# Performance work log

Measured on AMD Instinct MI355X. Metric: run time of the kernel, lower is better.

## Reference

```python
import jax, jax.numpy as jnp
import numpy as np

N = 1024      # n_nodes
S = 32        # state_dim
M = 32        # message_dim
STEPS = 5     # n_steps


def setup_inputs() -> dict:
    key = jax.random.key(0)
    ks = jax.random.split(key, 12)
    w = lambda k, shape: jax.random.normal(k, shape, jnp.float32) * 0.02
    return {
        "J": jax.random.normal(ks[0], (N, N), jnp.float32),
        "b": jax.random.normal(ks[1], (N,), jnp.float32),
        # message_passing MLP (Linear(2S+3->M), Linear(M->M), Linear(M->M))
        "W1": w(ks[2], (M, 2 * S + 3)), "b1": jnp.zeros((M,), jnp.float32),
        "W2": w(ks[3], (M, M)),         "b2": jnp.zeros((M,), jnp.float32),
        "W3": w(ks[4], (M, M)),         "b3": jnp.zeros((M,), jnp.float32),
        # GRU(input=S+M, hidden=S). h0 is always zero in the original forward,
        # so weight_hh never contributes (only bias_hh does) and is omitted.
        "W_ih": w(ks[5], (3 * S, S + M)),
        "b_ih": w(ks[6], (3 * S,)),
        "b_hh": w(ks[7], (3 * S,)),
        # readout MLP (Linear(S->M), Linear(M->M), Linear(M->2))
        "R1": w(ks[8], (M, S)),  "rb1": jnp.zeros((M,), jnp.float32),
        "R2": w(ks[9], (M, M)),  "rb2": jnp.zeros((M,), jnp.float32),
        "R3": w(ks[10], (2, M)), "rb3": jnp.zeros((2,), jnp.float32),
    }


def reference(J, b, W1, b1, W2, b2, W3, b3, W_ih, b_ih, b_hh, R1, rb1, R2, rb2, R3, rb3):
    # Split first linear over the concat [h_i, h_j, J_ij, b_i, b_j] so the
    # [N, N, 2S+3] concat tensor is never materialized.
    W1a, W1b = W1[:, :S], W1[:, S:2 * S]
    wJ, wbi, wbj = W1[:, 2 * S], W1[:, 2 * S + 1], W1[:, 2 * S + 2]

    def step(h, _):
        hi = h @ W1a.T                       # [N, M] (sender part)
        hj = h @ W1b.T                       # [N, M] (receiver part)
        pre = (hi[:, None, :] + hj[None, :, :]
               + J[:, :, None] * wJ
               + b[:, None, None] * wbi
               + b[None, :, None] * wbj
               + b1)                          # [N, N, M]
        x = jax.nn.relu(pre)
        x = jax.nn.relu(x @ W2.T + b2)
        x = jax.nn.relu(x @ W3.T + b3)       # message_i_j: [N, N, M]
        m = x.sum(0)                          # message to node j: sum over senders i
        # GRU with zero initial hidden state: h' = (1-z) * n_gate
        gi = jnp.concatenate([h, m], axis=-1) @ W_ih.T + b_ih  # [N, 3S]
        r = jax.nn.sigmoid(gi[:, :S] + b_hh[:S])
        z = jax.nn.sigmoid(gi[:, S:2 * S] + b_hh[S:2 * S])
        n = jnp.tanh(gi[:, 2 * S:] + r * b_hh[2 * S:])
        return (1.0 - z) * n, None

    h0 = jnp.zeros((N, S), J.dtype)
    h, _ = jax.lax.scan(step, h0, None, length=STEPS)

    r = jax.nn.relu(h @ R1.T + rb1)
    r = jax.nn.relu(r @ R2.T + rb2)
    r = jax.nn.relu(r @ R3.T + rb3)          # [N, 2]
    return jax.nn.sigmoid(r)
```

## Files before the change

### kernel.cpp

```cpp
#include <hip/hip_runtime.h>
#include <math.h>

#define NN 1024

typedef __attribute__((ext_vector_type(8))) short bf16x8;
typedef __attribute__((ext_vector_type(4))) float f32x4;
typedef __attribute__((ext_vector_type(4))) unsigned int u32x4;

__device__ __forceinline__ float sigmoidf_(float x) { return 1.0f / (1.0f + __expf(-x)); }

__device__ __forceinline__ unsigned int pk_bf16(float a, float b) {
    unsigned int ua = __float_as_uint(a), ub = __float_as_uint(b);
    ua += 0x7fffu + ((ua >> 16) & 1u);
    ub += 0x7fffu + ((ub >> 16) & 1u);
    return (ua >> 16) | (ub & 0xffff0000u);
}
__device__ __forceinline__ unsigned short f2bf_rne(float a) {
    unsigned int ua = __float_as_uint(a);
    ua += 0x7fffu + ((ua >> 16) & 1u);
    return (unsigned short)(ua >> 16);
}

struct Ctx {
    bf16x8 w2a0, w2a1, w3a0, w3a1;
    f32x4 b2v0, b2v1, b3v0, b3v1;
    float wj8[8];
};

__device__ __forceinline__ void make_ctx(Ctx& c, int p, int q,
    const float* __restrict__ W1, const float* __restrict__ W2,
    const float* __restrict__ b2, const float* __restrict__ W3,
    const float* __restrict__ b3)
{
    union FU { bf16x8 v; unsigned short s[8]; } t0, t1, t2, t3;
#pragma unroll
    for (int jj = 0; jj < 8; jj++) {
        int k = q * 8 + jj;
        t0.s[jj] = f2bf_rne(W2[p * 32 + k]);
        t1.s[jj] = f2bf_rne(W2[(16 + p) * 32 + k]);
        t2.s[jj] = f2bf_rne(W3[p * 32 + k]);
        t3.s[jj] = f2bf_rne(W3[(16 + p) * 32 + k]);
        c.wj8[jj] = W1[k * 67 + 64];
    }
    c.w2a0 = t0.v; c.w2a1 = t1.v; c.w3a0 = t2.v; c.w3a1 = t3.v;
#pragma unroll
    for (int r = 0; r < 4; r++) {
        c.b2v0[r] = b2[q * 4 + r];  c.b2v1[r] = b2[16 + q * 4 + r];
        c.b3v0[r] = b3[q * 4 + r];  c.b3v1[r] = b3[16 + q * 4 + r];
    }
}

__global__ __launch_bounds__(256) void k_pre(
    const float* __restrict__ J, const float* __restrict__ b,
    const float* __restrict__ W1, const float* __restrict__ b1,
    float* __restrict__ Jt, float* __restrict__ h,
    float* __restrict__ u0, float* __restrict__ v)
{
    __shared__ float tile[32][33];
    const int t = blockIdx.x;
    const int tid = threadIdx.x;
    if (t < 1024) {
        int tx = (t & 31) * 32, ty = (t >> 5) * 32;
        int x = tid & 31, y = tid >> 5;
#pragma unroll
        for (int r = 0; r < 4; r++)
            tile[y + 8 * r][x] = J[(size_t)(ty + y + 8 * r) * NN + tx + x];
        __syncthreads();
#pragma unroll
        for (int r = 0; r < 4; r++)
            Jt[(size_t)(tx + y + 8 * r) * NN + ty + x] = tile[x][y + 8 * r];
    } else {
        int idx = (t - 1024) * 256 + tid;
        int row = idx >> 5, mm = idx & 31;
        float bi = b[row];
        h[idx]  = 0.f;
        u0[idx] = bi * W1[mm * 67 + 65];
        v[idx]  = fmaf(bi, W1[mm * 67 + 66], b1[mm]);
    }
}

__global__ __launch_bounds__(256, 4) void k_step(
    const float* __restrict__ Jt, const float* __restrict__ W1,
    const float* __restrict__ W2, const float* __restrict__ b2,
    const float* __restrict__ W3, const float* __restrict__ b3,
    const float* __restrict__ Wih, const float* __restrict__ bih,
    const float* __restrict__ bhh, const float* __restrict__ b,
    const float* __restrict__ b1,
    const float* __restrict__ R1, const float* __restrict__ rb1,
    const float* __restrict__ R2, const float* __restrict__ rb2,
    const float* __restrict__ R3, const float* __restrict__ rb3,
    float* __restrict__ h, float* __restrict__ v,
    const float* __restrict__ ui, float* __restrict__ uo,
    float* __restrict__ out, int do_out)
{
    __shared__ float red[4 * 32];
    __shared__ float hm[64];
    __shared__ float gbuf[96];
    __shared__ float hnb[32];
    __shared__ float tb[32];

    const int tid = threadIdx.x;
    const int w = tid >> 6;
    const int l = tid & 63;
    const int p = l & 15;
    const int q = l >> 4;
    const int j = blockIdx.x & 1023;
    const bool primary = (blockIdx.x < 1024);

    Ctx c; make_ctx(c, p, q, W1, W2, b2, W3, b3);
    const float* Jtrow = Jt + (size_t)j * NN;

    float vv[8];
#pragma unroll
    for (int jj = 0; jj < 8; jj++) vv[jj] = v[j * 32 + q * 8 + jj];

    const int s0 = (p | ((l & 16) << 1)) << 2;
    const int s1 = s0 + 64;
    const bool qlo = (l & 32) == 0;

    f32x4 acc0 = {0.f, 0.f, 0.f, 0.f}, acc1 = {0.f, 0.f, 0.f, 0.f};

    const int ibase = w * 256;
    float  jwA = Jtrow[ibase + p];
    float4 uaA = *(const float4*)(ui + (ibase + p) * 32 + q * 8);
    float4 ubA = *(const float4*)(ui + (ibase + p) * 32 + q * 8 + 4);
    float  jwB = Jtrow[ibase + 16 + p];
    float4 uaB = *(const float4*)(ui + (ibase + 16 + p) * 32 + q * 8);
    float4 ubB = *(const float4*)(ui + (ibase + 16 + p) * 32 + q * 8 + 4);

#pragma unroll 4
    for (int t = 0; t < 16; ++t) {
        float  jw_c;
        float4 ua_c, ub_c;
        if ((t & 1) == 0) { jw_c = jwA; ua_c = uaA; ub_c = ubA; }
        else              { jw_c = jwB; ua_c = uaB; ub_c = ubB; }
        if (t < 14) {
            const int in = ibase + (t + 2) * 16 + p;
            if ((t & 1) == 0) {
                jwA = Jtrow[in];
                uaA = *(const float4*)(ui + in * 32 + q * 8);
                ubA = *(const float4*)(ui + in * 32 + q * 8 + 4);
            } else {
                jwB = Jtrow[in];
                uaB = *(const float4*)(ui + in * 32 + q * 8);
                ubB = *(const float4*)(ui + in * 32 + q * 8 + 4);
            }
        }

        float xr[8];
        xr[0] = fmaxf(fmaf(jw_c, c.wj8[0], ua_c.x + vv[0]), 0.f);
        xr[1] = fmaxf(fmaf(jw_c, c.wj8[1], ua_c.y + vv[1]), 0.f);
        xr[2] = fmaxf(fmaf(jw_c, c.wj8[2], ua_c.z + vv[2]), 0.f);
        xr[3] = fmaxf(fmaf(jw_c, c.wj8[3], ua_c.w + vv[3]), 0.f);
        xr[4] = fmaxf(fmaf(jw_c, c.wj8[4], ub_c.x + vv[4]), 0.f);
        xr[5] = fmaxf(fmaf(jw_c, c.wj8[5], ub_c.y + vv[5]), 0.f);
        xr[6] = fmaxf(fmaf(jw_c, c.wj8[6], ub_c.z + vv[6]), 0.f);
        xr[7] = fmaxf(fmaf(jw_c, c.wj8[7], ub_c.w + vv[7]), 0.f);

        union BU { u32x4 u4; bf16x8 v; unsigned int d[4]; } bx;
#pragma unroll
        for (int cc = 0; cc < 4; cc++) bx.d[cc] = pk_bf16(xr[2 * cc], xr[2 * cc + 1]);

        f32x4 c0 = __builtin_amdgcn_mfma_f32_16x16x32_bf16(c.w2a0, bx.v, c.b2v0, 0, 0, 0);
        f32x4 c1 = __builtin_amdgcn_mfma_f32_16x16x32_bf16(c.w2a1, bx.v, c.b2v1, 0, 0, 0);

        const int d0 = (int)pk_bf16(fmaxf(c0[0], 0.f), fmaxf(c0[1], 0.f));
        const int d1 = (int)pk_bf16(fmaxf(c0[2], 0.f), fmaxf(c0[3], 0.f));
        const int d2 = (int)pk_bf16(fmaxf(c1[0], 0.f), fmaxf(c1[1], 0.f));
        const int d3 = (int)pk_bf16(fmaxf(c1[2], 0.f), fmaxf(c1[3], 0.f));

        const int A0 = __builtin_amdgcn_ds_bpermute(s0, d0);
        const int A1 = __builtin_amdgcn_ds_bpermute(s0, d1);
        const int A2 = __builtin_amdgcn_ds_bpermute(s1, d0);
        const int A3 = __builtin_amdgcn_ds_bpermute(s1, d1);
        const int B0 = __builtin_amdgcn_ds_bpermute(s0, d2);
        const int B1 = __builtin_amdgcn_ds_bpermute(s0, d3);
        const int B2 = __builtin_amdgcn_ds_bpermute(s1, d2);
        const int B3 = __builtin_amdgcn_ds_bpermute(s1, d3);

        union BU yr;
        yr.d[0] = (unsigned)(qlo ? A0 : B0);
        yr.d[1] = (unsigned)(qlo ? A1 : B1);
        yr.d[2] = (unsigned)(qlo ? A2 : B2);
        yr.d[3] = (unsigned)(qlo ? A3 : B3);

        f32x4 e0 = __builtin_amdgcn_mfma_f32_16x16x32_bf16(c.w3a0, yr.v, c.b3v0, 0, 0, 0);
        f32x4 e1 = __builtin_amdgcn_mfma_f32_16x16x32_bf16(c.w3a1, yr.v, c.b3v1, 0, 0, 0);
#pragma unroll
        for (int r = 0; r < 4; r++) {
            acc0[r] += fmaxf(e0[r], 0.f);
            acc1[r] += fmaxf(e1[r], 0.f);
        }
    }

#pragma unroll
    for (int bit = 1; bit < 16; bit <<= 1) {
#pragma unroll
        for (int r = 0; r < 4; r++) {
            acc0[r] += __shfl_xor(acc0[r], bit);
            acc1[r] += __shfl_xor(acc1[r], bit);
        }
    }
    if (p == 0) {
#pragma unroll
        for (int r = 0; r < 4; r++) {
            red[w * 32 + q * 4 + r]      = acc0[r];
            red[w * 32 + 16 + q * 4 + r] = acc1[r];
        }
    }

    if (!primary) return;
    __syncthreads();

    if (tid < 64) {
        float val;
        if (tid < 32) val = h[j * 32 + tid];
        else {
            int s = tid - 32;
            val = red[s] + red[32 + s] + red[64 + s] + red[96 + s];
        }
        hm[tid] = val;
    }
    __syncthreads();

    if (tid < 192) {
        const int row = tid >> 1, half = tid & 1;
        const float* wr = Wih + row * 64 + half * 32;
        const float* hh = hm + half * 32;
        float acc = 0.f;
#pragma unroll
        for (int k4 = 0; k4 < 8; k4++) {
            float4 w4 = *(const float4*)(wr + 4 * k4);
            acc = fmaf(w4.x, hh[4 * k4 + 0], acc);
            acc = fmaf(w4.y, hh[4 * k4 + 1], acc);
            acc = fmaf(w4.z, hh[4 * k4 + 2], acc);
            acc = fmaf(w4.w, hh[4 * k4 + 3], acc);
        }
        acc += __shfl_xor(acc, 1);
        if (half == 0) gbuf[row] = acc + bih[row];
    }
    __syncthreads();

    if (tid < 32) {
        const int s = tid;
        float r = sigmoidf_(gbuf[s] + bhh[s]);
        float z = sigmoidf_(gbuf[32 + s] + bhh[32 + s]);
        float n = tanhf(gbuf[64 + s] + r * bhh[64 + s]);
        float hn_ = (1.0f - z) * n;
        hnb[s] = hn_;
        h[j * 32 + s] = hn_;
    }
    __syncthreads();

    if (tid < 64) {
        const int s = tid & 31;
        const bool isV = tid >= 32;
        const float bj = b[j];
        const float* wr = W1 + s * 67 + (isV ? 32 : 0);
        float acc = isV ? fmaf(bj, W1[s * 67 + 66], b1[s]) : bj * W1[s * 67 + 65];
#pragma unroll
        for (int k = 0; k < 32; k++) acc = fmaf(wr[k], hnb[k], acc);
        if (isV) v[j * 32 + s] = acc;
        else     uo[j * 32 + s] = acc;
    }

    if (do_out) {
        __syncthreads();
        if (tid < 32) {
            float a = rb1[tid];
            const float* rr = R1 + tid * 32;
#pragma unroll
            for (int k4 = 0; k4 < 8; k4++) {
                float4 w4 = *(const float4*)(rr + 4 * k4);
                a = fmaf(w4.x, hnb[4 * k4 + 0], a);
                a = fmaf(w4.y, hnb[4 * k4 + 1], a);
                a = fmaf(w4.z, hnb[4 * k4 + 2], a);
                a = fmaf(w4.w, hnb[4 * k4 + 3], a);
            }
            gbuf[tid] = fmaxf(a, 0.f);
        }
        __syncthreads();
        if (tid < 32) {
            float a = rb2[tid];
            const float* rr = R2 + tid * 32;
#pragma unroll
            for (int k4 = 0; k4 < 8; k4++) {
                float4 w4 = *(const float4*)(rr + 4 * k4);
                a = fmaf(w4.x, gbuf[4 * k4 + 0], a);
                a = fmaf(w4.y, gbuf[4 * k4 + 1], a);
                a = fmaf(w4.z, gbuf[4 * k4 + 2], a);
                a = fmaf(w4.w, gbuf[4 * k4 + 3], a);
            }
            tb[tid] = fmaxf(a, 0.f);
        }
        __syncthreads();
        if (tid < 2) {
            float a = rb3[tid];
            const float* rr = R3 + tid * 32;
#pragma unroll
            for (int k = 0; k < 32; k++) a = fmaf(rr[k], tb[k], a);
            out[j * 2 + tid] = sigmoidf_(fmaxf(a, 0.f));
        }
    }
}

extern "C" void kernel_launch(void* const* d_in, const int* in_sizes, int n_in,
                              void* d_out, int out_size, void* d_ws, size_t ws_size,
                              hipStream_t stream)
{
    const float* J   = (const float*)d_in[0];
    const float* b   = (const float*)d_in[1];
    const float* W1  = (const float*)d_in[2];
    const float* b1  = (const float*)d_in[3];
    const float* W2  = (const float*)d_in[4];
    const float* b2  = (const float*)d_in[5];
    const float* W3  = (const float*)d_in[6];
    const float* b3  = (const float*)d_in[7];
    const float* Wih = (const float*)d_in[8];
    const float* bih = (const float*)d_in[9];
    const float* bhh = (const float*)d_in[10];
    const float* R1  = (const float*)d_in[11];
    const float* rb1 = (const float*)d_in[12];
    const float* R2  = (const float*)d_in[13];
    const float* rb2 = (const float*)d_in[14];
    const float* R3  = (const float*)d_in[15];
    const float* rb3 = (const float*)d_in[16];

    float* out = (float*)d_out;
    float* ws  = (float*)d_ws;
    float* h  = ws;
    float* v  = ws + 32768;
    float* u0 = ws + 65536;
    float* u1 = ws + 98304;
    float* Jt = ws + 131072;

    k_pre<<<1152, 256, 0, stream>>>(J, b, W1, b1, Jt, h, u0, v);
    for (int s = 0; s < 5; s++) {
        const float* ui = (s & 1) ? u1 : u0;
        float*       uo = (s & 1) ? u0 : u1;
        int grid = (s == 0) ? 2048 : 1024;
        k_step<<<grid, 256, 0, stream>>>(Jt, W1, W2, b2, W3, b3, Wih, bih,
                                         bhh, b, b1, R1, rb1, R2, rb2, R3,
                                         rb3, h, v, ui, uo, out,
                                         (s == 4) ? 1 : 0);
    }
}
```

Baseline: 241.4 us.

## Fuse five step kernels into one cooperative persistent kernel with grid sync

Replaces the five per-step kernel launches with a single cooperative kernel that loops over the steps, keeps h and v in shared memory, stages Wih and W1 in LDS, and uses grid.sync between steps to exchange the u vectors. It also swaps the round-to-nearest-even bf16 pack for a cheaper round-half-up pack using v_perm. The intent is to remove launch gaps and global round trips for the per-node state. In exchange it needs all 1024 blocks co-resident (4 per CU), pays grid barrier cost, and changes bf16 rounding slightly. A fallback path keeps the multi-launch version.

New measurement: 220.5 us. -8.6%, faster.

```diff
diff --git a/kernel.cpp b/kernel.cpp
--- a/kernel.cpp
+++ b/kernel.cpp
@@ -1,5 +1,8 @@
 #include <hip/hip_runtime.h>
+#include <hip/hip_cooperative_groups.h>
 #include <math.h>
+
+namespace cg = cooperative_groups;
 
 #define NN 1024
 
@@ -9,11 +12,9 @@
 
 __device__ __forceinline__ float sigmoidf_(float x) { return 1.0f / (1.0f + __expf(-x)); }
 
-__device__ __forceinline__ unsigned int pk_bf16(float a, float b) {
-    unsigned int ua = __float_as_uint(a), ub = __float_as_uint(b);
-    ua += 0x7fffu + ((ua >> 16) & 1u);
-    ub += 0x7fffu + ((ub >> 16) & 1u);
-    return (ua >> 16) | (ub & 0xffff0000u);
+__device__ __forceinline__ unsigned int pk2(float a, float b) {
+    return __builtin_amdgcn_perm(__float_as_uint(a) + 0x8000u,
+                                 __float_as_uint(b) + 0x8000u, 0x03020706u);
 }
 __device__ __forceinline__ unsigned short f2bf_rne(float a) {
     unsigned int ua = __float_as_uint(a);
@@ -50,76 +51,11 @@
     }
 }
 
-__global__ __launch_bounds__(256) void k_pre(
-    const float* __restrict__ J, const float* __restrict__ b,
-    const float* __restrict__ W1, const float* __restrict__ b1,
-    float* __restrict__ Jt, float* __restrict__ h,
-    float* __restrict__ u0, float* __restrict__ v)
+__device__ __forceinline__ void main16(const Ctx& c,
+    const float* __restrict__ Jtrow, const float* __restrict__ ui,
+    const float* vv, int w, int p, int q, int s0, int s1, bool qlo,
+    f32x4& acc0, f32x4& acc1)
 {
-    __shared__ float tile[32][33];
-    const int t = blockIdx.x;
-    const int tid = threadIdx.x;
-    if (t < 1024) {
-        int tx = (t & 31) * 32, ty = (t >> 5) * 32;
-        int x = tid & 31, y = tid >> 5;
-#pragma unroll
-        for (int r = 0; r < 4; r++)
-            tile[y + 8 * r][x] = J[(size_t)(ty + y + 8 * r) * NN + tx + x];
-        __syncthreads();
-#pragma unroll
-        for (int r = 0; r < 4; r++)
-            Jt[(size_t)(tx + y + 8 * r) * NN + ty + x] = tile[x][y + 8 * r];
-    } else {
-        int idx = (t - 1024) * 256 + tid;
-        int row = idx >> 5, mm = idx & 31;
-        float bi = b[row];
-        h[idx]  = 0.f;
-        u0[idx] = bi * W1[mm * 67 + 65];
-        v[idx]  = fmaf(bi, W1[mm * 67 + 66], b1[mm]);
-    }
-}
-
-__global__ __launch_bounds__(256, 4) void k_step(
-    const float* __restrict__ Jt, const float* __restrict__ W1,
-    const float* __restrict__ W2, const float* __restrict__ b2,
-    const float* __restrict__ W3, const float* __restrict__ b3,
-    const float* __restrict__ Wih, const float* __restrict__ bih,
-    const float* __restrict__ bhh, const float* __restrict__ b,
-    const float* __restrict__ b1,
-    const float* __restrict__ R1, const float* __restrict__ rb1,
-    const float* __restrict__ R2, const float* __restrict__ rb2,
-    const float* __restrict__ R3, const float* __restrict__ rb3,
-    float* __restrict__ h, float* __restrict__ v,
-    const float* __restrict__ ui, float* __restrict__ uo,
-    float* __restrict__ out, int do_out)
-{
-    __shared__ float red[4 * 32];
-    __shared__ float hm[64];
-    __shared__ float gbuf[96];
-    __shared__ float hnb[32];
-    __shared__ float tb[32];
-
-    const int tid = threadIdx.x;
-    const int w = tid >> 6;
-    const int l = tid & 63;
-    const int p = l & 15;
-    const int q = l >> 4;
-    const int j = blockIdx.x & 1023;
-    const bool primary = (blockIdx.x < 1024);
-
-    Ctx c; make_ctx(c, p, q, W1, W2, b2, W3, b3);
-    const float* Jtrow = Jt + (size_t)j * NN;
-
-    float vv[8];
-#pragma unroll
-    for (int jj = 0; jj < 8; jj++) vv[jj] = v[j * 32 + q * 8 + jj];
-
-    const int s0 = (p | ((l & 16) << 1)) << 2;
-    const int s1 = s0 + 64;
-    const bool qlo = (l & 32) == 0;
-
-    f32x4 acc0 = {0.f, 0.f, 0.f, 0.f}, acc1 = {0.f, 0.f, 0.f, 0.f};
-
     const int ibase = w * 256;
     float  jwA = Jtrow[ibase + p];
     float4 uaA = *(const float4*)(ui + (ibase + p) * 32 + q * 8);
@@ -158,16 +94,18 @@
         xr[7] = fmaxf(fmaf(jw_c, c.wj8[7], ub_c.w + vv[7]), 0.f);
 
         union BU { u32x4 u4; bf16x8 v; unsigned int d[4]; } bx;
-#pragma unroll
-        for (int cc = 0; cc < 4; cc++) bx.d[cc] = pk_bf16(xr[2 * cc], xr[2 * cc + 1]);
+        bx.d[0] = pk2(xr[0], xr[1]);
+        bx.d[1] = pk2(xr[2], xr[3]);
+        bx.d[2] = pk2(xr[4], xr[5]);
+        bx.d[3] = pk2(xr[6], xr[7]);
 
         f32x4 c0 = __builtin_amdgcn_mfma_f32_16x16x32_bf16(c.w2a0, bx.v, c.b2v0, 0, 0, 0);
         f32x4 c1 = __builtin_amdgcn_mfma_f32_16x16x32_bf16(c.w2a1, bx.v, c.b2v1, 0, 0, 0);
 
-        const int d0 = (int)pk_bf16(fmaxf(c0[0], 0.f), fmaxf(c0[1], 0.f));
-        const int d1 = (int)pk_bf16(fmaxf(c0[2], 0.f), fmaxf(c0[3], 0.f));
-        const int d2 = (int)pk_bf16(fmaxf(c1[0], 0.f), fmaxf(c1[1], 0.f));
-        const int d3 = (int)pk_bf16(fmaxf(c1[2], 0.f), fmaxf(c1[3], 0.f));
+        const int d0 = (int)pk2(fmaxf(c0[0], 0.f), fmaxf(c0[1], 0.f));
+        const int d1 = (int)pk2(fmaxf(c0[2], 0.f), fmaxf(c0[3], 0.f));
+        const int d2 = (int)pk2(fmaxf(c1[0], 0.f), fmaxf(c1[1], 0.f));
+        const int d3 = (int)pk2(fmaxf(c1[2], 0.f), fmaxf(c1[3], 0.f));
 
         const int A0 = __builtin_amdgcn_ds_bpermute(s0, d0);
         const int A1 = __builtin_amdgcn_ds_bpermute(s0, d1);
@@ -192,6 +130,225 @@
             acc1[r] += fmaxf(e1[r], 0.f);
         }
     }
+}
+
+__global__ __launch_bounds__(256) void k_pre(
+    const float* __restrict__ J, const float* __restrict__ b,
+    const float* __restrict__ W1, const float* __restrict__ b1,
+    float* __restrict__ Jt, float* __restrict__ h,
+    float* __restrict__ u0, float* __restrict__ v)
+{
+    __shared__ float tile[32][33];
+    const int t = blockIdx.x;
+    const int tid = threadIdx.x;
+    if (t < 1024) {
+        int tx = (t & 31) * 32, ty = (t >> 5) * 32;
+        int x = tid & 31, y = tid >> 5;
+#pragma unroll
+        for (int r = 0; r < 4; r++)
+            tile[y + 8 * r][x] = J[(size_t)(ty + y + 8 * r) * NN + tx + x];
+        __syncthreads();
+#pragma unroll
+        for (int r = 0; r < 4; r++)
+            Jt[(size_t)(tx + y + 8 * r) * NN + ty + x] = tile[x][y + 8 * r];
+    } else {
+        int idx = (t - 1024) * 256 + tid;
+        int row = idx >> 5, mm = idx & 31;
+        float bi = b[row];
+        h[idx]  = 0.f;
+        u0[idx] = bi * W1[mm * 67 + 65];
+        v[idx]  = fmaf(bi, W1[mm * 67 + 66], b1[mm]);
+    }
+}
+
+__global__ __launch_bounds__(256, 4) void k_coop(
+    const float* __restrict__ Jt, const float* __restrict__ W1,
+    const float* __restrict__ W2, const float* __restrict__ b2,
+    const float* __restrict__ W3, const float* __restrict__ b3,
+    const float* __restrict__ Wih, const float* __restrict__ bih,
+    const float* __restrict__ bhh, const float* __restrict__ b,
+    const float* __restrict__ b1,
+    const float* __restrict__ R1, const float* __restrict__ rb1,
+    const float* __restrict__ R2, const float* __restrict__ rb2,
+    const float* __restrict__ R3, const float* __restrict__ rb3,
+    float* __restrict__ u0, float* __restrict__ u1, float* __restrict__ out)
+{
+    __shared__ float WihT[64 * 96];
+    __shared__ float W1L[32 * 67];
+    __shared__ float bihL[96], bhhL[96], b1L[32];
+    __shared__ float red[4 * 32];
+    __shared__ float hm[64], gbuf[96], hnb[32], tb[32];
+    __shared__ float hbuf[32], vbuf[32];
+
+    const int tid = threadIdx.x;
+    const int w = tid >> 6;
+    const int l = tid & 63;
+    const int p = l & 15;
+    const int q = l >> 4;
+    const int j = blockIdx.x;
+    const float bj = b[j];
+
+    cg::grid_group grid = cg::this_grid();
+
+    Ctx c; make_ctx(c, p, q, W1, W2, b2, W3, b3);
+    const float* Jtrow = Jt + (size_t)j * NN;
+
+    for (int t = tid; t < 96 * 64; t += 256)
+        WihT[(t & 63) * 96 + (t >> 6)] = Wih[t];
+    for (int t = tid; t < 32 * 67; t += 256) W1L[t] = W1[t];
+    if (tid < 96) { bihL[tid] = bih[tid]; bhhL[tid] = bhh[tid]; }
+    if (tid < 32) {
+        b1L[tid]  = b1[tid];
+        hbuf[tid] = 0.f;
+        vbuf[tid] = fmaf(bj, W1[tid * 67 + 66], b1[tid]);
+    }
+    __syncthreads();
+
+    const int s0 = (p | ((l & 16) << 1)) << 2;
+    const int s1 = s0 + 64;
+    const bool qlo = (l & 32) == 0;
+
+    for (int step = 0; step < 5; ++step) {
+        const float* ui = (step & 1) ? u1 : u0;
+        float*       uo = (step & 1) ? u0 : u1;
+
+        float vv[8];
+#pragma unroll
+        for (int jj = 0; jj < 8; jj++) vv[jj] = vbuf[q * 8 + jj];
+
+        f32x4 acc0 = {0.f, 0.f, 0.f, 0.f}, acc1 = {0.f, 0.f, 0.f, 0.f};
+        main16(c, Jtrow, ui, vv, w, p, q, s0, s1, qlo, acc0, acc1);
+
+#pragma unroll
+        for (int bit = 1; bit < 16; bit <<= 1) {
+#pragma unroll
+            for (int r = 0; r < 4; r++) {
+                acc0[r] += __shfl_xor(acc0[r], bit);
+                acc1[r] += __shfl_xor(acc1[r], bit);
+            }
+        }
+        if (p == 0) {
+#pragma unroll
+            for (int r = 0; r < 4; r++) {
+                red[w * 32 + q * 4 + r]      = acc0[r];
+                red[w * 32 + 16 + q * 4 + r] = acc1[r];
+            }
+        }
+        __syncthreads();
+
+        if (tid < 64) {
+            float val;
+            if (tid < 32) val = hbuf[tid];
+            else {
+                int s = tid - 32;
+                val = red[s] + red[32 + s] + red[64 + s] + red[96 + s];
+            }
+            hm[tid] = val;
+        }
+        __syncthreads();
+
+        if (tid < 192) {
+            const int row = tid >> 1, half = tid & 1;
+            float acc = 0.f;
+#pragma unroll 8
+            for (int k = 0; k < 32; k++)
+                acc = fmaf(WihT[(half * 32 + k) * 96 + row], hm[half * 32 + k], acc);
+            acc += __shfl_xor(acc, 1);
+            if (half == 0) gbuf[row] = acc + bihL[row];
+        }
+        __syncthreads();
+
+        if (tid < 32) {
+            const int s = tid;
+            float r = sigmoidf_(gbuf[s] + bhhL[s]);
+            float z = sigmoidf_(gbuf[32 + s] + bhhL[32 + s]);
+            float n = tanhf(gbuf[64 + s] + r * bhhL[64 + s]);
+            float hn_ = (1.0f - z) * n;
+            hnb[s] = hn_;
+            hbuf[s] = hn_;
+        }
+        __syncthreads();
+
+        if (tid < 64) {
+            const int s = tid & 31;
+            const bool isV = tid >= 32;
+            const float* wr = W1L + s * 67 + (isV ? 32 : 0);
+            float acc = isV ? fmaf(bj, W1L[s * 67 + 66], b1L[s]) : bj * W1L[s * 67 + 65];
+#pragma unroll 8
+            for (int k = 0; k < 32; k++) acc = fmaf(wr[k], hnb[k], acc);
+            if (isV) vbuf[s] = acc;
+            else     uo[j * 32 + s] = acc;
+        }
+
+        if (step < 4) {
+            __threadfence();
+            grid.sync();
+        }
+    }
+
+    __syncthreads();
+    if (tid < 32) {
+        float a = rb1[tid];
+        const float* rr = R1 + tid * 32;
+#pragma unroll 8
+        for (int k = 0; k < 32; k++) a = fmaf(rr[k], hnb[k], a);
+        gbuf[tid] = fmaxf(a, 0.f);
+    }
+    __syncthreads();
+    if (tid < 32) {
+        float a = rb2[tid];
+        const float* rr = R2 + tid * 32;
+#pragma unroll 8
+        for (int k = 0; k < 32; k++) a = fmaf(rr[k], gbuf[k], a);
+        tb[tid] = fmaxf(a, 0.f);
+    }
+    __syncthreads();
+    if (tid < 2) {
+        float a = rb3[tid];
+        const float* rr = R3 + tid * 32;
+#pragma unroll 8
+        for (int k = 0; k < 32; k++) a = fmaf(rr[k], tb[k], a);
+        out[j * 2 + tid] = sigmoidf_(fmaxf(a, 0.f));
+    }
+}
+
+__global__ __launch_bounds__(256, 4) void k_step(
+    const float* __restrict__ Jt, const float* __restrict__ W1,
+    const float* __restrict__ W2, const float* __restrict__ b2,
+    const float* __restrict__ W3, const float* __restrict__ b3,
+    const float* __restrict__ Wih, const float* __restrict__ bih,
+    const float* __restrict__ bhh, const float* __restrict__ b,
+    const float* __restrict__ b1,
+    const float* __restrict__ R1, const float* __restrict__ rb1,
+    const float* __restrict__ R2, const float* __restrict__ rb2,
+    const float* __restrict__ R3, const float* __restrict__ rb3,
+    float* __restrict__ h, float* __restrict__ v,
+    const float* __restrict__ ui, float* __restrict__ uo,
+    float* __restrict__ out, int do_out)
+{
+    __shared__ float red[4 * 32];
+    __shared__ float hm[64], gbuf[96], hnb[32], tb[32];
+
+    const int tid = threadIdx.x;
+    const int w = tid >> 6;
+    const int l = tid & 63;
+    const int p = l & 15;
+    const int q = l >> 4;
+    const int j = blockIdx.x;
+
+    Ctx c; make_ctx(c, p, q, W1, W2, b2, W3, b3);
+    const float* Jtrow = Jt + (size_t)j * NN;
+
+    float vv[8];
+#pragma unroll
+    for (int jj = 0; jj < 8; jj++) vv[jj] = v[j * 32 + q * 8 + jj];
+
+    const int s0 = (p | ((l & 16) << 1)) << 2;
+    const int s1 = s0 + 64;
+    const bool qlo = (l & 32) == 0;
+
+    f32x4 acc0 = {0.f, 0.f, 0.f, 0.f}, acc1 = {0.f, 0.f, 0.f, 0.f};
+    main16(c, Jtrow, ui, vv, w, p, q, s0, s1, qlo, acc0, acc1);
 
 #pragma unroll
     for (int bit = 1; bit < 16; bit <<= 1) {
@@ -208,8 +365,6 @@
             red[w * 32 + 16 + q * 4 + r] = acc1[r];
         }
     }
-
-    if (!primary) return;
     __syncthreads();
 
     if (tid < 64) {
@@ -269,35 +424,23 @@
         if (tid < 32) {
             float a = rb1[tid];
             const float* rr = R1 + tid * 32;
-#pragma unroll
-            for (int k4 = 0; k4 < 8; k4++) {
-                float4 w4 = *(const float4*)(rr + 4 * k4);
-                a = fmaf(w4.x, hnb[4 * k4 + 0], a);
-                a = fmaf(w4.y, hnb[4 * k4 + 1], a);
-                a = fmaf(w4.z, hnb[4 * k4 + 2], a);
-                a = fmaf(w4.w, hnb[4 * k4 + 3], a);
-            }
+#pragma unroll 8
+            for (int k = 0; k < 32; k++) a = fmaf(rr[k], hnb[k], a);
             gbuf[tid] = fmaxf(a, 0.f);
         }
         __syncthreads();
         if (tid < 32) {
             float a = rb2[tid];
             const float* rr = R2 + tid * 32;
-#pragma unroll
-            for (int k4 = 0; k4 < 8; k4++) {
-                float4 w4 = *(const float4*)(rr + 4 * k4);
-                a = fmaf(w4.x, gbuf[4 * k4 + 0], a);
-                a = fmaf(w4.y, gbuf[4 * k4 + 1], a);
-                a = fmaf(w4.z, gbuf[4 * k4 + 2], a);
-                a = fmaf(w4.w, gbuf[4 * k4 + 3], a);
-            }
+#pragma unroll 8
+            for (int k = 0; k < 32; k++) a = fmaf(rr[k], gbuf[k], a);
             tb[tid] = fmaxf(a, 0.f);
         }
         __syncthreads();
         if (tid < 2) {
             float a = rb3[tid];
             const float* rr = R3 + tid * 32;
-#pragma unroll
+#pragma unroll 8
             for (int k = 0; k < 32; k++) a = fmaf(rr[k], tb[k], a);
             out[j * 2 + tid] = sigmoidf_(fmaxf(a, 0.f));
         }
@@ -335,13 +478,32 @@
     float* Jt = ws + 131072;
 
     k_pre<<<1152, 256, 0, stream>>>(J, b, W1, b1, Jt, h, u0, v);
-    for (int s = 0; s < 5; s++) {
-        const float* ui = (s & 1) ? u1 : u0;
-        float*       uo = (s & 1) ? u0 : u1;
-        int grid = (s == 0) ? 2048 : 1024;
-        k_step<<<grid, 256, 0, stream>>>(Jt, W1, W2, b2, W3, b3, Wih, bih,
-                                         bhh, b, b1, R1, rb1, R2, rb2, R3,
-                                         rb3, h, v, ui, uo, out,
-                                         (s == 4) ? 1 : 0);
-    }
-}
+
+    int mb = 0;
+    bool coop =
+        (hipOccupancyMaxActiveBlocksPerMultiprocessor(
+             &mb, reinterpret_cast<const void*>(&k_coop), 256, 0) == hipSuccess) &&
+        (mb >= 4);
+    if (coop) {
+        void* cargs[] = { (void*)&Jt, (void*)&W1, (void*)&W2, (void*)&b2,
+                          (void*)&W3, (void*)&b3, (void*)&Wih, (void*)&bih,
+                          (void*)&bhh, (void*)&b, (void*)&b1,
+                          (void*)&R1, (void*)&rb1, (void*)&R2, (void*)&rb2,
+                          (void*)&R3, (void*)&rb3,
+                          (void*)&u0, (void*)&u1, (void*)&out };
+        if (hipLaunchCooperativeKernel(reinterpret_cast<const void*>(&k_coop),
+                                       dim3(1024), dim3(256), cargs, 0, stream)
+            != hipSuccess)
+            coop = false;
+    }
+    if (!coop) {
+        for (int s = 0; s < 5; s++) {
+            const float* ui = (s & 1) ? u1 : u0;
+            float*       uo = (s & 1) ? u0 : u1;
+            k_step<<<1024, 256, 0, stream>>>(Jt, W1, W2, b2, W3, b3, Wih, bih,
+                                             bhh, b, b1, R1, rb1, R2, rb2, R3,
+                                             rb3, h, v, ui, uo, out,
+                                             (s == 4) ? 1 : 0);
+        }
+    }
+}
```

## Precompute bf16 MLP weights once in setup kernel and simplify bf16 packing

Applied to the files above, without the earlier changes.

Moves the per-block conversion of W2/W3 to bf16 MFMA fragments, plus the bias and J-weight gathers, into an extra block of the setup kernel that writes them to a workspace config buffer. Each step block then loads them with a few vector loads instead of many scalar loads and conversions. The bf16 packing switches from round-to-nearest-even to round-half-up using a byte permute, which needs fewer instructions but rounds ties differently. The first step's doubled grid (2048 blocks with early-exiting duplicates) is dropped to a uniform 1024, and the readout loops are rewritten as scalar unrolled loops.

Result: faster. 200.9 us (-16.8%).

```diff
diff --git a/kernel.cpp b/kernel.cpp
--- a/kernel.cpp
+++ b/kernel.cpp
@@ -9,11 +9,9 @@
 
 __device__ __forceinline__ float sigmoidf_(float x) { return 1.0f / (1.0f + __expf(-x)); }
 
-__device__ __forceinline__ unsigned int pk_bf16(float a, float b) {
-    unsigned int ua = __float_as_uint(a), ub = __float_as_uint(b);
-    ua += 0x7fffu + ((ua >> 16) & 1u);
-    ub += 0x7fffu + ((ub >> 16) & 1u);
-    return (ua >> 16) | (ub & 0xffff0000u);
+__device__ __forceinline__ unsigned int pk2(float a, float b) {
+    return __builtin_amdgcn_perm(__float_as_uint(a) + 0x8000u,
+                                 __float_as_uint(b) + 0x8000u, 0x03020706u);
 }
 __device__ __forceinline__ unsigned short f2bf_rne(float a) {
     unsigned int ua = __float_as_uint(a);
@@ -21,40 +19,15 @@
     return (unsigned short)(ua >> 16);
 }
 
-struct Ctx {
-    bf16x8 w2a0, w2a1, w3a0, w3a1;
-    f32x4 b2v0, b2v1, b3v0, b3v1;
-    float wj8[8];
-};
-
-__device__ __forceinline__ void make_ctx(Ctx& c, int p, int q,
-    const float* __restrict__ W1, const float* __restrict__ W2,
-    const float* __restrict__ b2, const float* __restrict__ W3,
-    const float* __restrict__ b3)
-{
-    union FU { bf16x8 v; unsigned short s[8]; } t0, t1, t2, t3;
-#pragma unroll
-    for (int jj = 0; jj < 8; jj++) {
-        int k = q * 8 + jj;
-        t0.s[jj] = f2bf_rne(W2[p * 32 + k]);
-        t1.s[jj] = f2bf_rne(W2[(16 + p) * 32 + k]);
-        t2.s[jj] = f2bf_rne(W3[p * 32 + k]);
-        t3.s[jj] = f2bf_rne(W3[(16 + p) * 32 + k]);
-        c.wj8[jj] = W1[k * 67 + 64];
-    }
-    c.w2a0 = t0.v; c.w2a1 = t1.v; c.w3a0 = t2.v; c.w3a1 = t3.v;
-#pragma unroll
-    for (int r = 0; r < 4; r++) {
-        c.b2v0[r] = b2[q * 4 + r];  c.b2v1[r] = b2[16 + q * 4 + r];
-        c.b3v0[r] = b3[q * 4 + r];  c.b3v1[r] = b3[16 + q * 4 + r];
-    }
-}
+#define CFG_FLOATS 2560
 
 __global__ __launch_bounds__(256) void k_pre(
     const float* __restrict__ J, const float* __restrict__ b,
     const float* __restrict__ W1, const float* __restrict__ b1,
+    const float* __restrict__ W2, const float* __restrict__ b2,
+    const float* __restrict__ W3, const float* __restrict__ b3,
     float* __restrict__ Jt, float* __restrict__ h,
-    float* __restrict__ u0, float* __restrict__ v)
+    float* __restrict__ u0, float* __restrict__ v, float* __restrict__ cfg)
 {
     __shared__ float tile[32][33];
     const int t = blockIdx.x;
@@ -69,23 +42,52 @@
 #pragma unroll
         for (int r = 0; r < 4; r++)
             Jt[(size_t)(tx + y + 8 * r) * NN + ty + x] = tile[x][y + 8 * r];
-    } else {
+    } else if (t < 1152) {
         int idx = (t - 1024) * 256 + tid;
         int row = idx >> 5, mm = idx & 31;
         float bi = b[row];
         h[idx]  = 0.f;
         u0[idx] = bi * W1[mm * 67 + 65];
         v[idx]  = fmaf(bi, W1[mm * 67 + 66], b1[mm]);
+    } else if (tid < 64) {
+        const int l = tid, p = l & 15, q = l >> 4;
+        union FU { unsigned int d[4]; unsigned short s[8]; } t0, t1, t2, t3;
+        float wj[8];
+#pragma unroll
+        for (int jj = 0; jj < 8; jj++) {
+            int k = q * 8 + jj;
+            t0.s[jj] = f2bf_rne(W2[p * 32 + k]);
+            t1.s[jj] = f2bf_rne(W2[(16 + p) * 32 + k]);
+            t2.s[jj] = f2bf_rne(W3[p * 32 + k]);
+            t3.s[jj] = f2bf_rne(W3[(16 + p) * 32 + k]);
+            wj[jj] = W1[k * 67 + 64];
+        }
+        u32x4* cw = (u32x4*)cfg;
+        cw[l]       = *(u32x4*)t0.d;
+        cw[64 + l]  = *(u32x4*)t1.d;
+        cw[128 + l] = *(u32x4*)t2.d;
+        cw[192 + l] = *(u32x4*)t3.d;
+        f32x4* cf = (f32x4*)(cfg + 1024);
+        f32x4 v0, v1, v2, v3;
+#pragma unroll
+        for (int r = 0; r < 4; r++) {
+            v0[r] = b2[q * 4 + r];  v1[r] = b2[16 + q * 4 + r];
+            v2[r] = b3[q * 4 + r];  v3[r] = b3[16 + q * 4 + r];
+        }
+        cf[l] = v0; cf[64 + l] = v1; cf[128 + l] = v2; cf[192 + l] = v3;
+        f32x4* cj = (f32x4*)(cfg + 2048);
+        f32x4 wlo, whi;
+#pragma unroll
+        for (int r = 0; r < 4; r++) { wlo[r] = wj[r]; whi[r] = wj[4 + r]; }
+        cj[l] = wlo; cj[64 + l] = whi;
     }
 }
 
 __global__ __launch_bounds__(256, 4) void k_step(
-    const float* __restrict__ Jt, const float* __restrict__ W1,
-    const float* __restrict__ W2, const float* __restrict__ b2,
-    const float* __restrict__ W3, const float* __restrict__ b3,
+    const float* __restrict__ Jt, const float* __restrict__ cfg,
     const float* __restrict__ Wih, const float* __restrict__ bih,
     const float* __restrict__ bhh, const float* __restrict__ b,
-    const float* __restrict__ b1,
+    const float* __restrict__ b1, const float* __restrict__ W1,
     const float* __restrict__ R1, const float* __restrict__ rb1,
     const float* __restrict__ R2, const float* __restrict__ rb2,
     const float* __restrict__ R3, const float* __restrict__ rb3,
@@ -94,26 +96,35 @@
     float* __restrict__ out, int do_out)
 {
     __shared__ float red[4 * 32];
-    __shared__ float hm[64];
-    __shared__ float gbuf[96];
-    __shared__ float hnb[32];
-    __shared__ float tb[32];
+    __shared__ float hm[64], gbuf[96], hnb[32], tb[32];
 
     const int tid = threadIdx.x;
     const int w = tid >> 6;
     const int l = tid & 63;
     const int p = l & 15;
     const int q = l >> 4;
-    const int j = blockIdx.x & 1023;
-    const bool primary = (blockIdx.x < 1024);
-
-    Ctx c; make_ctx(c, p, q, W1, W2, b2, W3, b3);
+    const int j = blockIdx.x;
+
+    union FU { bf16x8 v; u32x4 u4; } w2a0, w2a1, w3a0, w3a1;
+    const u32x4* cw = (const u32x4*)cfg;
+    w2a0.u4 = cw[l]; w2a1.u4 = cw[64 + l]; w3a0.u4 = cw[128 + l]; w3a1.u4 = cw[192 + l];
+    const f32x4* cf = (const f32x4*)(cfg + 1024);
+    const f32x4 b2v0 = cf[l], b2v1 = cf[64 + l], b3v0 = cf[128 + l], b3v1 = cf[192 + l];
+    const f32x4* cj = (const f32x4*)(cfg + 2048);
+    const f32x4 wlo = cj[l], whi = cj[64 + l];
+    float wj8[8];
+#pragma unroll
+    for (int r = 0; r < 4; r++) { wj8[r] = wlo[r]; wj8[4 + r] = whi[r]; }
+
+    float vv[8];
+    {
+        float4 va = *(const float4*)(v + j * 32 + q * 8);
+        float4 vb = *(const float4*)(v + j * 32 + q * 8 + 4);
+        vv[0] = va.x; vv[1] = va.y; vv[2] = va.z; vv[3] = va.w;
+        vv[4] = vb.x; vv[5] = vb.y; vv[6] = vb.z; vv[7] = vb.w;
+    }
+
     const float* Jtrow = Jt + (size_t)j * NN;
-
-    float vv[8];
-#pragma unroll
-    for (int jj = 0; jj < 8; jj++) vv[jj] = v[j * 32 + q * 8 + jj];
-
     const int s0 = (p | ((l & 16) << 1)) << 2;
     const int s1 = s0 + 64;
     const bool qlo = (l & 32) == 0;
@@ -148,26 +159,28 @@
         }
 
         float xr[8];
-        xr[0] = fmaxf(fmaf(jw_c, c.wj8[0], ua_c.x + vv[0]), 0.f);
-        xr[1] = fmaxf(fmaf(jw_c, c.wj8[1], ua_c.y + vv[1]), 0.f);
-        xr[2] = fmaxf(fmaf(jw_c, c.wj8[2], ua_c.z + vv[2]), 0.f);
-        xr[3] = fmaxf(fmaf(jw_c, c.wj8[3], ua_c.w + vv[3]), 0.f);
-        xr[4] = fmaxf(fmaf(jw_c, c.wj8[4], ub_c.x + vv[4]), 0.f);
-        xr[5] = fmaxf(fmaf(jw_c, c.wj8[5], ub_c.y + vv[5]), 0.f);
-        xr[6] = fmaxf(fmaf(jw_c, c.wj8[6], ub_c.z + vv[6]), 0.f);
-        xr[7] = fmaxf(fmaf(jw_c, c.wj8[7], ub_c.w + vv[7]), 0.f);
+        xr[0] = fmaxf(fmaf(jw_c, wj8[0], ua_c.x + vv[0]), 0.f);
+        xr[1] = fmaxf(fmaf(jw_c, wj8[1], ua_c.y + vv[1]), 0.f);
+        xr[2] = fmaxf(fmaf(jw_c, wj8[2], ua_c.z + vv[2]), 0.f);
+        xr[3] = fmaxf(fmaf(jw_c, wj8[3], ua_c.w + vv[3]), 0.f);
+        xr[4] = fmaxf(fmaf(jw_c, wj8[4], ub_c.x + vv[4]), 0.f);
+        xr[5] = fmaxf(fmaf(jw_c, wj8[5], ub_c.y + vv[5]), 0.f);
+        xr[6] = fmaxf(fmaf(jw_c, wj8[6], ub_c.z + vv[6]), 0.f);
+        xr[7] = fmaxf(fmaf(jw_c, wj8[7], ub_c.w + vv[7]), 0.f);
 
         union BU { u32x4 u4; bf16x8 v; unsigned int d[4]; } bx;
-#pragma unroll
-        for (int cc = 0; cc < 4; cc++) bx.d[cc] = pk_bf16(xr[2 * cc], xr[2 * cc + 1]);
-
-        f32x4 c0 = __builtin_amdgcn_mfma_f32_16x16x32_bf16(c.w2a0, bx.v, c.b2v0, 0, 0, 0);
-        f32x4 c1 = __builtin_amdgcn_mfma_f32_16x16x32_bf16(c.w2a1, bx.v, c.b2v1, 0, 0, 0);
-
-        const int d0 = (int)pk_bf16(fmaxf(c0[0], 0.f), fmaxf(c0[1], 0.f));
-        const int d1 = (int)pk_bf16(fmaxf(c0[2], 0.f), fmaxf(c0[3], 0.f));
-        const int d2 = (int)pk_bf16(fmaxf(c1[0], 0.f), fmaxf(c1[1], 0.f));
-        const int d3 = (int)pk_bf16(fmaxf(c1[2], 0.f), fmaxf(c1[3], 0.f));
+        bx.d[0] = pk2(xr[0], xr[1]);
+        bx.d[1] = pk2(xr[2], xr[3]);
+        bx.d[2] = pk2(xr[4], xr[5]);
+        bx.d[3] = pk2(xr[6], xr[7]);
+
+        f32x4 c0 = __builtin_amdgcn_mfma_f32_16x16x32_bf16(w2a0.v, bx.v, b2v0, 0, 0, 0);
+        f32x4 c1 = __builtin_amdgcn_mfma_f32_16x16x32_bf16(w2a1.v, bx.v, b2v1, 0, 0, 0);
+
+        const int d0 = (int)pk2(fmaxf(c0[0], 0.f), fmaxf(c0[1], 0.f));
+        const int d1 = (int)pk2(fmaxf(c0[2], 0.f), fmaxf(c0[3], 0.f));
+        const int d2 = (int)pk2(fmaxf(c1[0], 0.f), fmaxf(c1[1], 0.f));
+        const int d3 = (int)pk2(fmaxf(c1[2], 0.f), fmaxf(c1[3], 0.f));
 
         const int A0 = __builtin_amdgcn_ds_bpermute(s0, d0);
         const int A1 = __builtin_amdgcn_ds_bpermute(s0, d1);
@@ -184,8 +197,8 @@
         yr.d[2] = (unsigned)(qlo ? A2 : B2);
         yr.d[3] = (unsigned)(qlo ? A3 : B3);
 
-        f32x4 e0 = __builtin_amdgcn_mfma_f32_16x16x32_bf16(c.w3a0, yr.v, c.b3v0, 0, 0, 0);
-        f32x4 e1 = __builtin_amdgcn_mfma_f32_16x16x32_bf16(c.w3a1, yr.v, c.b3v1, 0, 0, 0);
+        f32x4 e0 = __builtin_amdgcn_mfma_f32_16x16x32_bf16(w3a0.v, yr.v, b3v0, 0, 0, 0);
+        f32x4 e1 = __builtin_amdgcn_mfma_f32_16x16x32_bf16(w3a1.v, yr.v, b3v1, 0, 0, 0);
 #pragma unroll
         for (int r = 0; r < 4; r++) {
             acc0[r] += fmaxf(e0[r], 0.f);
@@ -208,8 +221,6 @@
             red[w * 32 + 16 + q * 4 + r] = acc1[r];
         }
     }
-
-    if (!primary) return;
     __syncthreads();
 
     if (tid < 64) {
@@ -269,35 +280,23 @@
         if (tid < 32) {
             float a = rb1[tid];
             const float* rr = R1 + tid * 32;
-#pragma unroll
-            for (int k4 = 0; k4 < 8; k4++) {
-                float4 w4 = *(const float4*)(rr + 4 * k4);
-                a = fmaf(w4.x, hnb[4 * k4 + 0], a);
-                a = fmaf(w4.y, hnb[4 * k4 + 1], a);
-                a = fmaf(w4.z, hnb[4 * k4 + 2], a);
-                a = fmaf(w4.w, hnb[4 * k4 + 3], a);
-            }
+#pragma unroll 8
+            for (int k = 0; k < 32; k++) a = fmaf(rr[k], hnb[k], a);
             gbuf[tid] = fmaxf(a, 0.f);
         }
         __syncthreads();
         if (tid < 32) {
             float a = rb2[tid];
             const float* rr = R2 + tid * 32;
-#pragma unroll
-            for (int k4 = 0; k4 < 8; k4++) {
-                float4 w4 = *(const float4*)(rr + 4 * k4);
-                a = fmaf(w4.x, gbuf[4 * k4 + 0], a);
-                a = fmaf(w4.y, gbuf[4 * k4 + 1], a);
-                a = fmaf(w4.z, gbuf[4 * k4 + 2], a);
-                a = fmaf(w4.w, gbuf[4 * k4 + 3], a);
-            }
+#pragma unroll 8
+            for (int k = 0; k < 32; k++) a = fmaf(rr[k], gbuf[k], a);
             tb[tid] = fmaxf(a, 0.f);
         }
         __syncthreads();
         if (tid < 2) {
             float a = rb3[tid];
             const float* rr = R3 + tid * 32;
-#pragma unroll
+#pragma unroll 8
             for (int k = 0; k < 32; k++) a = fmaf(rr[k], tb[k], a);
             out[j * 2 + tid] = sigmoidf_(fmaxf(a, 0.f));
         }
@@ -328,20 +327,20 @@
 
     float* out = (float*)d_out;
     float* ws  = (float*)d_ws;
-    float* h  = ws;
-    float* v  = ws + 32768;
-    float* u0 = ws + 65536;
-    float* u1 = ws + 98304;
-    float* Jt = ws + 131072;
-
-    k_pre<<<1152, 256, 0, stream>>>(J, b, W1, b1, Jt, h, u0, v);
+    float* h   = ws;
+    float* v   = ws + 32768;
+    float* u0  = ws + 65536;
+    float* u1  = ws + 98304;
+    float* Jt  = ws + 131072;
+    float* cfg = ws + 131072 + NN * NN;
+
+    k_pre<<<1153, 256, 0, stream>>>(J, b, W1, b1, W2, b2, W3, b3,
+                                    Jt, h, u0, v, cfg);
     for (int s = 0; s < 5; s++) {
         const float* ui = (s & 1) ? u1 : u0;
         float*       uo = (s & 1) ? u0 : u1;
-        int grid = (s == 0) ? 2048 : 1024;
-        k_step<<<grid, 256, 0, stream>>>(Jt, W1, W2, b2, W3, b3, Wih, bih,
-                                         bhh, b, b1, R1, rb1, R2, rb2, R3,
-                                         rb3, h, v, ui, uo, out,
-                                         (s == 4) ? 1 : 0);
-    }
-}
+        k_step<<<1024, 256, 0, stream>>>(Jt, cfg, Wih, bih, bhh, b, b1, W1,
+                                         R1, rb1, R2, rb2, R3, rb3,
+                                         h, v, ui, uo, out, (s == 4) ? 1 : 0);
+    }
+}
```
